# Kernel tuning notes

Measured on AMD Instinct MI355X. Metric: run time of the kernel, lower is better.

## Reference

```python
import jax, jax.numpy as jnp
import numpy as np

N_LAYER = 4
N_EMBD = 768
N_HEAD = 12
B, T = 4, 1024  # T = 4 * t, t = 256 (block_size)
EPS = 1e-5


def layernorm(x, g, b):
    mu = jnp.mean(x, axis=-1, keepdims=True)
    var = jnp.var(x, axis=-1, keepdims=True)
    return (x - mu) * jax.lax.rsqrt(var + EPS) * g + b


def setup_inputs() -> dict:
    key = jax.random.key(0)
    ks = jax.random.split(key, 20)
    C, L, H = N_EMBD, N_LAYER, 4 * N_EMBD
    std = 0.02
    inp = {
        "x": jax.random.normal(ks[0], (B, T, C), dtype=jnp.float32),
        "ln1_g": jnp.ones((L, C), jnp.float32),
        "ln1_b": jnp.zeros((L, C), jnp.float32),
        "Wq": std * jax.random.normal(ks[1], (L, C, C), jnp.float32),
        "bq": jnp.zeros((L, C), jnp.float32),
        "Wk": std * jax.random.normal(ks[2], (L, C, C), jnp.float32),
        "bk": jnp.zeros((L, C), jnp.float32),
        "Wv": std * jax.random.normal(ks[3], (L, C, C), jnp.float32),
        "bv": jnp.zeros((L, C), jnp.float32),
        "Wp": std * jax.random.normal(ks[4], (L, C, C), jnp.float32),
        "bp": jnp.zeros((L, C), jnp.float32),
        "ln2_g": jnp.ones((L, C), jnp.float32),
        "ln2_b": jnp.zeros((L, C), jnp.float32),
        "W1": std * jax.random.normal(ks[5], (L, C, H), jnp.float32),
        "b1": jnp.zeros((L, H), jnp.float32),
        "W2": std * jax.random.normal(ks[6], (L, H, C), jnp.float32),
        "b2": jnp.zeros((L, C), jnp.float32),
    }
    return inp


def _forward(x, ln1_g, ln1_b, Wq, bq, Wk, bk, Wv, bv, Wp, bp, ln2_g, ln2_b, W1, b1, W2, b2):
    Bx, Tx, C = x.shape
    hd = C // N_HEAD
    t = Tx // 4
    # cross-conditional mask: causal tril(t,t) tiled 4x4 over the 4 streams
    mask = jnp.tile(jnp.tril(jnp.ones((t, t), dtype=bool)), (4, 4))  # [T, T]
    scale = 1.0 / np.sqrt(hd).astype(np.float32)

    def block(h, p):
        (g1, b1g, wq, bqv, wk, bkv, wv, bvv, wp, bpv, g2, b2g, w1, b1v, w2, b2v) = p
        a_in = layernorm(h, g1, b1g)
        q = (a_in @ wq + bqv).reshape(Bx, Tx, N_HEAD, hd).transpose(0, 2, 1, 3)
        k = (a_in @ wk + bkv).reshape(Bx, Tx, N_HEAD, hd).transpose(0, 2, 1, 3)
        v = (a_in @ wv + bvv).reshape(Bx, Tx, N_HEAD, hd).transpose(0, 2, 1, 3)
        att = jnp.einsum('bhqd,bhkd->bhqk', q, k) * scale
        att = jnp.where(mask, att, -jnp.inf)
        att = jax.nn.softmax(att, axis=-1)
        y = jnp.einsum('bhqk,bhkd->bhqd', att, v)
        y = y.transpose(0, 2, 1, 3).reshape(Bx, Tx, C)
        h = h + (y @ wp + bpv)
        m_in = layernorm(h, g2, b2g)
        m = jax.nn.gelu(m_in @ w1 + b1v, approximate=False) @ w2 + b2v
        return h + m, None

    params = (ln1_g, ln1_b, Wq, bq, Wk, bk, Wv, bv, Wp, bp, ln2_g, ln2_b, W1, b1, W2, b2)
    x, _ = jax.lax.scan(block, x, params)
    return x


def reference(x, ln1_g, ln1_b, Wq, bq, Wk, bk, Wv, bv, Wp, bp, ln2_g, ln2_b, W1, b1, W2, b2):
    return _forward(x, ln1_g, ln1_b, Wq, bq, Wk, bk, Wv, bv, Wp, bp, ln2_g, ln2_b, W1, b1, W2, b2)
```

## Files before the change

### kernel.cpp

```cpp
#include <hip/hip_runtime.h>
#include <hip/hip_bf16.h>
#include <math.h>

typedef __hip_bfloat16 bf16;
typedef __attribute__((ext_vector_type(8))) short bf16x8;
typedef __attribute__((ext_vector_type(4))) float f32x4;

#define CDIM 768
#define HDIM 64
#define NHEAD 12
#define TSEQ 1024
#define MROWS 4096
#define HID 3072
#define QKVN 2304

__device__ inline void gld16(const void* g, void* l) {
  __builtin_amdgcn_global_load_lds((const __attribute__((address_space(1))) void*)g,
                                   (__attribute__((address_space(3))) void*)l, 16, 0, 0);
}

__global__ void k_transall(const float* __restrict__ Wq, const float* __restrict__ Wk,
                           const float* __restrict__ Wv, const float* __restrict__ Wp,
                           const float* __restrict__ W1, const float* __restrict__ W2,
                           const float* __restrict__ bq, const float* __restrict__ bk,
                           const float* __restrict__ bv,
                           bf16* __restrict__ wqkv, bf16* __restrict__ wtp,
                           bf16* __restrict__ wt1, bf16* __restrict__ wt2,
                           float* __restrict__ bqkv) {
  __shared__ float t[32][33];
  int blk = blockIdx.x;
  if (blk >= 6912) {
    int i = (blk - 6912) * 256 + threadIdx.y * 32 + threadIdx.x;
    if (i < QKVN) bqkv[i] = (i < CDIM) ? bq[i] : (i < 2 * CDIM) ? bk[i - CDIM] : bv[i - 2 * CDIM];
    return;
  }
  const float* src; bf16* dst; int K, N, n0, k0;
  if (blk < 1728) {
    int w = blk / 576, id = blk % 576;
    src = (w == 0) ? Wq : (w == 1) ? Wk : Wv;
    dst = wqkv + (size_t)w * CDIM * CDIM;
    K = CDIM; N = CDIM;
    n0 = (id % 24) * 32; k0 = (id / 24) * 32;
  } else if (blk < 2304) {
    int id = blk - 1728;
    src = Wp; dst = wtp; K = CDIM; N = CDIM;
    n0 = (id % 24) * 32; k0 = (id / 24) * 32;
  } else if (blk < 4608) {
    int id = blk - 2304;
    src = W1; dst = wt1; K = CDIM; N = HID;
    n0 = (id % 96) * 32; k0 = (id / 96) * 32;
  } else {
    int id = blk - 4608;
    src = W2; dst = wt2; K = HID; N = CDIM;
    n0 = (id % 24) * 32; k0 = (id / 24) * 32;
  }
  int c = threadIdx.x, ry = threadIdx.y;
  #pragma unroll
  for (int i = 0; i < 4; i++) {
    int r = ry + 8 * i;
    t[r][c] = src[(size_t)(k0 + r) * N + n0 + c];
  }
  __syncthreads();
  #pragma unroll
  for (int i = 0; i < 4; i++) {
    int r = ry + 8 * i;
    dst[(size_t)(n0 + r) * K + k0 + c] = __float2bfloat16(t[c][r]);
  }
}

__global__ __launch_bounds__(256) void k_ln(const float* __restrict__ h, const float* __restrict__ g,
                                            const float* __restrict__ b, bf16* __restrict__ out) {
  int row = blockIdx.x, tid = threadIdx.x;
  const float* hr = h + (size_t)row * CDIM;
  float x0 = hr[tid], x1 = hr[tid + 256], x2 = hr[tid + 512];
  float s = x0 + x1 + x2;
  float ss = x0 * x0 + x1 * x1 + x2 * x2;
  #pragma unroll
  for (int off = 32; off > 0; off >>= 1) {
    s  += __shfl_down(s, off, 64);
    ss += __shfl_down(ss, off, 64);
  }
  __shared__ float rs[4], rq[4];
  if ((tid & 63) == 0) { rs[tid >> 6] = s; rq[tid >> 6] = ss; }
  __syncthreads();
  s  = rs[0] + rs[1] + rs[2] + rs[3];
  ss = rq[0] + rq[1] + rq[2] + rq[3];
  float mu = s * (1.0f / CDIM);
  float var = ss * (1.0f / CDIM) - mu * mu;
  float rstd = rsqrtf(var + 1e-5f);
  bf16* orow = out + (size_t)row * CDIM;
  orow[tid]       = __float2bfloat16((x0 - mu) * rstd * g[tid]       + b[tid]);
  orow[tid + 256] = __float2bfloat16((x1 - mu) * rstd * g[tid + 256] + b[tid + 256]);
  orow[tid + 512] = __float2bfloat16((x2 - mu) * rstd * g[tid + 512] + b[tid + 512]);
}


template <int BM, int BN, int EPI>
__global__ __launch_bounds__(256) void k_gemmT(const bf16* __restrict__ A, const bf16* __restrict__ Bt,
                                               const float* __restrict__ bias,
                                               void* __restrict__ outv, int M, int N, int K) {
  constexpr int MR = BM / 32, NR = BN / 32;
  __shared__ __align__(16) bf16 As[BM * 64];
  __shared__ __align__(16) bf16 Bs[BN * 64];
  int tid = threadIdx.x;
  int m0 = blockIdx.x * BM, n0 = blockIdx.y * BN;
  int wave = tid >> 6, lane = tid & 63;
  int wr = wave >> 1, wc = wave & 1;
  int lrow = lane & 15, quad = lane >> 4;
  int sw = lrow & 7;
  f32x4 zz = {0.f, 0.f, 0.f, 0.f};
  f32x4 acc[MR][NR];
  #pragma unroll
  for (int i = 0; i < MR; i++)
    #pragma unroll
    for (int j = 0; j < NR; j++) acc[i][j] = zz;
  const bf16* Ag = A + (size_t)m0 * K;
  const bf16* Bg = Bt + (size_t)n0 * K;
  for (int k0 = 0; k0 < K; k0 += 64) {
    __syncthreads();
    #pragma unroll
    for (int i = 0; i < BM / 32; i++) {
      int idx = i * 256 + tid;
      int row = idx >> 3, c = idx & 7;
      gld16(Ag + (size_t)row * K + k0 + ((c ^ (row & 7)) * 8), As + idx * 8);
    }
    #pragma unroll
    for (int i = 0; i < BN / 32; i++) {
      int idx = i * 256 + tid;
      int row = idx >> 3, c = idx & 7;
      gld16(Bg + (size_t)row * K + k0 + ((c ^ (row & 7)) * 8), Bs + idx * 8);
    }
    __syncthreads();
    #pragma unroll
    for (int kc = 0; kc < 2; kc++) {
      int g = kc * 4 + quad;
      bf16x8 af[MR], bfr[NR];
      #pragma unroll
      for (int mi = 0; mi < MR; mi++)
        af[mi] = *(const bf16x8*)(As + (wr * (BM / 2) + mi * 16 + lrow) * 64 + ((g ^ sw) * 8));
      #pragma unroll
      for (int ni = 0; ni < NR; ni++)
        bfr[ni] = *(const bf16x8*)(Bs + (wc * (BN / 2) + ni * 16 + lrow) * 64 + ((g ^ sw) * 8));
      #pragma unroll
      for (int mi = 0; mi < MR; mi++)
        #pragma unroll
        for (int ni = 0; ni < NR; ni++)
          acc[mi][ni] = __builtin_amdgcn_mfma_f32_16x16x32_bf16(af[mi], bfr[ni], acc[mi][ni], 0, 0, 0);
    }
  }
  #pragma unroll
  for (int ni = 0; ni < NR; ni++) {
    int gc = n0 + wc * (BN / 2) + ni * 16 + lrow;
    float bval = bias[gc];
    #pragma unroll
    for (int mi = 0; mi < MR; mi++) {
      #pragma unroll
      for (int r = 0; r < 4; r++) {
        int grow = m0 + wr * (BM / 2) + mi * 16 + quad * 4 + r;
        float vv = acc[mi][ni][r] + bval;
        if (EPI == 1) vv = 0.5f * vv * (1.0f + erff(vv * 0.70710678118654752f));
        if (EPI == 2) {
          float* hp = (float*)outv + (size_t)grow * N + gc;
          *hp = *hp + vv;
        } else {
          ((bf16*)outv)[(size_t)grow * N + gc] = __float2bfloat16(vv);
        }
      }
    }
  }
}

__global__ __launch_bounds__(256) void k_attn(const bf16* __restrict__ qkv, bf16* __restrict__ y) {
  int bh = blockIdx.x;
  int b = bh / NHEAD, hh = bh % NHEAD;
  int qc = blockIdx.y;
  int tid = threadIdx.x;
  int wave = tid >> 6, lane = tid & 63;
  int lrow = lane & 15, quad = lane >> 4;
  int sw = lrow & 7;
  int q0 = qc * 64 + wave * 16;
  int qmod = q0 & 255;
  int qcmod = (qc * 64) & 255;

  const size_t rstride = QKVN;
  const bf16* qbase = qkv + (size_t)(b * TSEQ) * rstride + hh * HDIM;
  const bf16* kbase = qbase + CDIM;
  const bf16* vbase = qbase + 2 * CDIM;

  bf16x8 qf[2];
  #pragma unroll
  for (int kc = 0; kc < 2; kc++)
    qf[kc] = *(const bf16x8*)(qbase + (size_t)(q0 + lrow) * rstride + kc * 32 + quad * 8);

  f32x4 zz = {0.f, 0.f, 0.f, 0.f};
  f32x4 Oacc[4];
  #pragma unroll
  for (int j = 0; j < 4; j++) Oacc[j] = zz;
  float m[4] = {-1e30f, -1e30f, -1e30f, -1e30f};
  float l[4] = {0.f, 0.f, 0.f, 0.f};

  __shared__ __align__(16) bf16 Ks[64 * 64];
  __shared__ __align__(16) bf16 Vt[64 * 72];
  __shared__ __align__(16) bf16 Pl[4][16 * 64];

  for (int kt = 0; kt < 16; kt++) {
    int k0 = kt * 64;
    int kmod = k0 & 255;
    if (kmod > qcmod + 63) continue;
    __syncthreads();
    #pragma unroll
    for (int i = 0; i < 2; i++) {
      int idx = i * 256 + tid;
      int key = idx >> 3, c = idx & 7;
      gld16(kbase + (size_t)(k0 + key) * rstride + ((c ^ (key & 7)) * 8), Ks + idx * 8);
      int vkey = idx & 63, vd0 = (idx >> 6) * 8;
      bf16x8 vv = *(const bf16x8*)(vbase + (size_t)(k0 + vkey) * rstride + vd0);
      const bf16* vp = (const bf16*)&vv;
      #pragma unroll
      for (int j = 0; j < 8; j++) Vt[(vd0 + j) * 72 + vkey] = vp[j];
    }
    __syncthreads();
    if (kmod > qmod + 15) continue;

    f32x4 s[4];
    #pragma unroll
    for (int sub = 0; sub < 4; sub++) {
      s[sub] = zz;
      #pragma unroll
      for (int kc = 0; kc < 2; kc++) {
        int g = kc * 4 + quad;
        bf16x8 kf = *(const bf16x8*)(Ks + (sub * 16 + lrow) * 64 + ((g ^ sw) * 8));
        s[sub] = __builtin_amdgcn_mfma_f32_16x16x32_bf16(qf[kc], kf, s[sub], 0, 0, 0);
      }
    }
    bool partial = (kmod + 63 > qmod);
    #pragma unroll
    for (int sub = 0; sub < 4; sub++)
      #pragma unroll
      for (int r = 0; r < 4; r++) {
        float sv = s[sub][r] * 0.125f;
        if (partial) {
          int krel = kmod + sub * 16 + lrow;
          int qrel = qmod + quad * 4 + r;
          if (krel > qrel) sv = -1e30f;
        }
        s[sub][r] = sv;
      }
    float pr[4][4], alpha[4];
    #pragma unroll
    for (int r = 0; r < 4; r++) {
      float v = fmaxf(fmaxf(s[0][r], s[1][r]), fmaxf(s[2][r], s[3][r]));
      v = fmaxf(v, __shfl_xor(v, 1, 64));
      v = fmaxf(v, __shfl_xor(v, 2, 64));
      v = fmaxf(v, __shfl_xor(v, 4, 64));
      v = fmaxf(v, __shfl_xor(v, 8, 64));
      float mnew = fmaxf(m[r], v);
      alpha[r] = __expf(m[r] - mnew);
      m[r] = mnew;
      float rsum = 0.f;
      #pragma unroll
      for (int sub = 0; sub < 4; sub++) {
        pr[sub][r] = __expf(s[sub][r] - mnew);
        rsum += pr[sub][r];
      }
      rsum += __shfl_xor(rsum, 1, 64);
      rsum += __shfl_xor(rsum, 2, 64);
      rsum += __shfl_xor(rsum, 4, 64);
      rsum += __shfl_xor(rsum, 8, 64);
      l[r] = l[r] * alpha[r] + rsum;
    }
    #pragma unroll
    for (int j = 0; j < 4; j++)
      #pragma unroll
      for (int r = 0; r < 4; r++) Oacc[j][r] *= alpha[r];
    bf16* Pw = (bf16*)Pl[wave];
    #pragma unroll
    for (int sub = 0; sub < 4; sub++) {
      int cc = sub * 2 + (lrow >> 3);
      int e = lrow & 7;
      #pragma unroll
      for (int r = 0; r < 4; r++) {
        int mm = quad * 4 + r;
        Pw[mm * 64 + ((cc ^ (mm & 7)) * 8) + e] = __float2bfloat16(pr[sub][r]);
      }
    }
    bf16x8 pf[2];
    #pragma unroll
    for (int kc = 0; kc < 2; kc++) {
      int g = kc * 4 + quad;
      pf[kc] = *(const bf16x8*)(Pw + lrow * 64 + ((g ^ sw) * 8));
    }
    #pragma unroll
    for (int j = 0; j < 4; j++)
      #pragma unroll
      for (int kc = 0; kc < 2; kc++) {
        bf16x8 vf = *(const bf16x8*)(Vt + (j * 16 + lrow) * 72 + kc * 32 + quad * 8);
        Oacc[j] = __builtin_amdgcn_mfma_f32_16x16x32_bf16(pf[kc], vf, Oacc[j], 0, 0, 0);
      }
  }
  #pragma unroll
  for (int r = 0; r < 4; r++) {
    float inv = 1.0f / l[r];
    bf16* yp = y + (size_t)(b * TSEQ + q0 + quad * 4 + r) * CDIM + hh * HDIM;
    #pragma unroll
    for (int j = 0; j < 4; j++)
      yp[j * 16 + lrow] = __float2bfloat16(Oacc[j][r] * inv);
  }
}

extern "C" void kernel_launch(void* const* d_in, const int* in_sizes, int n_in,
                              void* d_out, int out_size, void* d_ws, size_t ws_size,
                              hipStream_t stream) {
  const float* x    = (const float*)d_in[0];
  const float* ln1g = (const float*)d_in[1];
  const float* ln1b = (const float*)d_in[2];
  const float* Wq   = (const float*)d_in[3];
  const float* bq   = (const float*)d_in[4];
  const float* Wk   = (const float*)d_in[5];
  const float* bk   = (const float*)d_in[6];
  const float* Wv   = (const float*)d_in[7];
  const float* bv   = (const float*)d_in[8];
  const float* Wp   = (const float*)d_in[9];
  const float* bp   = (const float*)d_in[10];
  const float* ln2g = (const float*)d_in[11];
  const float* ln2b = (const float*)d_in[12];
  const float* W1   = (const float*)d_in[13];
  const float* b1   = (const float*)d_in[14];
  const float* W2   = (const float*)d_in[15];
  const float* b2   = (const float*)d_in[16];

  char* ws = (char*)d_ws;
  size_t off = 0;
  float* h    = (float*)(ws + off); off += (size_t)MROWS * CDIM * 4;
  bf16* a     = (bf16*)(ws + off);  off += (size_t)MROWS * CDIM * 2;
  bf16* qkvb  = (bf16*)(ws + off);  off += (size_t)MROWS * QKVN * 2;
  bf16* yb    = (bf16*)(ws + off);  off += (size_t)MROWS * CDIM * 2;
  bf16* m1    = qkvb;
  bf16* wqkv  = (bf16*)(ws + off);  off += (size_t)QKVN * CDIM * 2;
  bf16* wtp   = (bf16*)(ws + off);  off += (size_t)CDIM * CDIM * 2;
  bf16* wt1   = (bf16*)(ws + off);  off += (size_t)CDIM * HID * 2;
  bf16* wt2   = (bf16*)(ws + off);  off += (size_t)CDIM * HID * 2;
  float* bqkv = (float*)(ws + off); off += (size_t)QKVN * 4;

  int n = MROWS * CDIM;
  hipMemcpyAsync(h, x, (size_t)n * sizeof(float), hipMemcpyDeviceToDevice, stream);

  for (int l = 0; l < 4; l++) {
    const float* Wql = Wq + (size_t)l * CDIM * CDIM;
    const float* Wkl = Wk + (size_t)l * CDIM * CDIM;
    const float* Wvl = Wv + (size_t)l * CDIM * CDIM;
    const float* Wpl = Wp + (size_t)l * CDIM * CDIM;
    const float* W1l = W1 + (size_t)l * CDIM * HID;
    const float* W2l = W2 + (size_t)l * HID * CDIM;

    k_transall<<<dim3(6921), dim3(32, 8), 0, stream>>>(Wql, Wkl, Wvl, Wpl, W1l, W2l,
                                                       bq + l * CDIM, bk + l * CDIM, bv + l * CDIM,
                                                       wqkv, wtp, wt1, wt2, bqkv);

    k_ln<<<dim3(MROWS), dim3(256), 0, stream>>>(h, ln1g + l * CDIM, ln1b + l * CDIM, a);

    k_gemmT<128, 128, 0><<<dim3(MROWS / 128, QKVN / 128), dim3(256), 0, stream>>>(
        a, wqkv, bqkv, qkvb, MROWS, QKVN, CDIM);

    k_attn<<<dim3(4 * NHEAD, 16), dim3(256), 0, stream>>>(qkvb, yb);

    k_gemmT<64, 64, 2><<<dim3(MROWS / 64, CDIM / 64), dim3(256), 0, stream>>>(
        yb, wtp, bp + (size_t)l * CDIM, h, MROWS, CDIM, CDIM);

    k_ln<<<dim3(MROWS), dim3(256), 0, stream>>>(h, ln2g + l * CDIM, ln2b + l * CDIM, a);

    k_gemmT<128, 128, 1><<<dim3(MROWS / 128, HID / 128), dim3(256), 0, stream>>>(
        a, wt1, b1 + (size_t)l * HID, m1, MROWS, HID, CDIM);

    k_gemmT<64, 64, 2><<<dim3(MROWS / 64, CDIM / 64), dim3(256), 0, stream>>>(
        m1, wt2, b2 + (size_t)l * CDIM, h, MROWS, CDIM, HID);
  }

  hipMemcpyAsync(d_out, h, (size_t)n * sizeof(float), hipMemcpyDeviceToDevice, stream);
}
```

Measured before the change: 928.2 us.

## Hoist weight transposes into one launch, vectorize layernorm, shrink GEMM M-tile

All four layers' weight transpose and bf16 conversion now run in a single launch before the layer loop when workspace allows, replacing one launch per layer. Layernorm now handles one row per wave with float4 loads and shuffle-xor reductions, dropping the shared-memory reduction and block sync. The QKV and MLP-up GEMMs switch from 128x128 to 64x128 tiles, doubling block count for better CU occupancy. The cost is more workspace for per-layer transposed weights and smaller tiles with less operand reuse.

Result: faster. 881.1 us (-5.1%).

```diff
diff --git a/kernel.cpp b/kernel.cpp
--- a/kernel.cpp
+++ b/kernel.cpp
@@ -4,6 +4,7 @@
 
 typedef __hip_bfloat16 bf16;
 typedef __attribute__((ext_vector_type(8))) short bf16x8;
+typedef __attribute__((ext_vector_type(4))) short s16x4;
 typedef __attribute__((ext_vector_type(4))) float f32x4;
 
 #define CDIM 768
@@ -18,17 +19,26 @@
   __builtin_amdgcn_global_load_lds((const __attribute__((address_space(1))) void*)g,
                                    (__attribute__((address_space(3))) void*)l, 16, 0, 0);
 }
-
-__global__ void k_transall(const float* __restrict__ Wq, const float* __restrict__ Wk,
-                           const float* __restrict__ Wv, const float* __restrict__ Wp,
-                           const float* __restrict__ W1, const float* __restrict__ W2,
-                           const float* __restrict__ bq, const float* __restrict__ bk,
-                           const float* __restrict__ bv,
-                           bf16* __restrict__ wqkv, bf16* __restrict__ wtp,
-                           bf16* __restrict__ wt1, bf16* __restrict__ wt2,
-                           float* __restrict__ bqkv) {
+__device__ inline short f2bs(float f) { bf16 h = __float2bfloat16(f); return *reinterpret_cast<short*>(&h); }
+
+__global__ void k_trans(const float* __restrict__ Wq, const float* __restrict__ Wk,
+                        const float* __restrict__ Wv, const float* __restrict__ Wp,
+                        const float* __restrict__ W1, const float* __restrict__ W2,
+                        const float* __restrict__ bq, const float* __restrict__ bk,
+                        const float* __restrict__ bv,
+                        bf16* __restrict__ wqkv, bf16* __restrict__ wtp,
+                        bf16* __restrict__ wt1, bf16* __restrict__ wt2,
+                        float* __restrict__ bqkv) {
   __shared__ float t[32][33];
   int blk = blockIdx.x;
+  int l = blk / 6921; blk -= l * 6921;
+  Wq += (size_t)l * CDIM * CDIM; Wk += (size_t)l * CDIM * CDIM;
+  Wv += (size_t)l * CDIM * CDIM; Wp += (size_t)l * CDIM * CDIM;
+  W1 += (size_t)l * CDIM * HID;  W2 += (size_t)l * HID * CDIM;
+  bq += (size_t)l * CDIM; bk += (size_t)l * CDIM; bv += (size_t)l * CDIM;
+  wqkv += (size_t)l * QKVN * CDIM; wtp += (size_t)l * CDIM * CDIM;
+  wt1  += (size_t)l * CDIM * HID;  wt2 += (size_t)l * CDIM * HID;
+  bqkv += (size_t)l * QKVN;
   if (blk >= 6912) {
     int i = (blk - 6912) * 256 + threadIdx.y * 32 + threadIdx.x;
     if (i < QKVN) bqkv[i] = (i < CDIM) ? bq[i] : (i < 2 * CDIM) ? bk[i - CDIM] : bv[i - 2 * CDIM];
@@ -70,28 +80,38 @@
 
 __global__ __launch_bounds__(256) void k_ln(const float* __restrict__ h, const float* __restrict__ g,
                                             const float* __restrict__ b, bf16* __restrict__ out) {
-  int row = blockIdx.x, tid = threadIdx.x;
-  const float* hr = h + (size_t)row * CDIM;
-  float x0 = hr[tid], x1 = hr[tid + 256], x2 = hr[tid + 512];
-  float s = x0 + x1 + x2;
-  float ss = x0 * x0 + x1 * x1 + x2 * x2;
+  int wave = threadIdx.x >> 6, lane = threadIdx.x & 63;
+  int row = blockIdx.x * 4 + wave;
+  const float4* hr = (const float4*)(h + (size_t)row * CDIM);
+  float4 v[3];
+  float s = 0.f, ss = 0.f;
+  #pragma unroll
+  for (int i = 0; i < 3; i++) {
+    v[i] = hr[lane * 3 + i];
+    s  += v[i].x + v[i].y + v[i].z + v[i].w;
+    ss += v[i].x * v[i].x + v[i].y * v[i].y + v[i].z * v[i].z + v[i].w * v[i].w;
+  }
   #pragma unroll
   for (int off = 32; off > 0; off >>= 1) {
-    s  += __shfl_down(s, off, 64);
-    ss += __shfl_down(ss, off, 64);
-  }
-  __shared__ float rs[4], rq[4];
-  if ((tid & 63) == 0) { rs[tid >> 6] = s; rq[tid >> 6] = ss; }
-  __syncthreads();
-  s  = rs[0] + rs[1] + rs[2] + rs[3];
-  ss = rq[0] + rq[1] + rq[2] + rq[3];
+    s  += __shfl_xor(s, off, 64);
+    ss += __shfl_xor(ss, off, 64);
+  }
   float mu = s * (1.0f / CDIM);
   float var = ss * (1.0f / CDIM) - mu * mu;
   float rstd = rsqrtf(var + 1e-5f);
-  bf16* orow = out + (size_t)row * CDIM;
-  orow[tid]       = __float2bfloat16((x0 - mu) * rstd * g[tid]       + b[tid]);
-  orow[tid + 256] = __float2bfloat16((x1 - mu) * rstd * g[tid + 256] + b[tid + 256]);
-  orow[tid + 512] = __float2bfloat16((x2 - mu) * rstd * g[tid + 512] + b[tid + 512]);
+  const float4* gp = (const float4*)g;
+  const float4* bp = (const float4*)b;
+  s16x4* orow = (s16x4*)(out + (size_t)row * CDIM);
+  #pragma unroll
+  for (int i = 0; i < 3; i++) {
+    float4 gg = gp[lane * 3 + i], bb = bp[lane * 3 + i];
+    s16x4 o;
+    o.x = f2bs((v[i].x - mu) * rstd * gg.x + bb.x);
+    o.y = f2bs((v[i].y - mu) * rstd * gg.y + bb.y);
+    o.z = f2bs((v[i].z - mu) * rstd * gg.z + bb.z);
+    o.w = f2bs((v[i].w - mu) * rstd * gg.w + bb.w);
+    orow[lane * 3 + i] = o;
+  }
 }
 
 
@@ -336,44 +356,61 @@
   bf16* qkvb  = (bf16*)(ws + off);  off += (size_t)MROWS * QKVN * 2;
   bf16* yb    = (bf16*)(ws + off);  off += (size_t)MROWS * CDIM * 2;
   bf16* m1    = qkvb;
-  bf16* wqkv  = (bf16*)(ws + off);  off += (size_t)QKVN * CDIM * 2;
-  bf16* wtp   = (bf16*)(ws + off);  off += (size_t)CDIM * CDIM * 2;
-  bf16* wt1   = (bf16*)(ws + off);  off += (size_t)CDIM * HID * 2;
-  bf16* wt2   = (bf16*)(ws + off);  off += (size_t)CDIM * HID * 2;
-  float* bqkv = (float*)(ws + off); off += (size_t)QKVN * 4;
+
+  const size_t szQkv = (size_t)QKVN * CDIM * 2;
+  const size_t szP   = (size_t)CDIM * CDIM * 2;
+  const size_t szW1  = (size_t)CDIM * HID * 2;
+  const size_t szW2  = (size_t)CDIM * HID * 2;
+  const size_t szB   = (size_t)QKVN * 4;
+  const size_t wlayer = szQkv + szP + szW1 + szW2 + szB;
+  bool hoist = ws_size >= off + 4 * wlayer + 4096;
+  int nW = hoist ? 4 : 1;
+
+  bf16* wqkv  = (bf16*)(ws + off);  off += nW * szQkv;
+  bf16* wtp   = (bf16*)(ws + off);  off += nW * szP;
+  bf16* wt1   = (bf16*)(ws + off);  off += nW * szW1;
+  bf16* wt2   = (bf16*)(ws + off);  off += nW * szW2;
+  float* bqkv = (float*)(ws + off); off += nW * szB;
 
   int n = MROWS * CDIM;
   hipMemcpyAsync(h, x, (size_t)n * sizeof(float), hipMemcpyDeviceToDevice, stream);
 
+  if (hoist)
+    k_trans<<<dim3(4 * 6921), dim3(32, 8), 0, stream>>>(Wq, Wk, Wv, Wp, W1, W2, bq, bk, bv,
+                                                        wqkv, wtp, wt1, wt2, bqkv);
+
   for (int l = 0; l < 4; l++) {
-    const float* Wql = Wq + (size_t)l * CDIM * CDIM;
-    const float* Wkl = Wk + (size_t)l * CDIM * CDIM;
-    const float* Wvl = Wv + (size_t)l * CDIM * CDIM;
-    const float* Wpl = Wp + (size_t)l * CDIM * CDIM;
-    const float* W1l = W1 + (size_t)l * CDIM * HID;
-    const float* W2l = W2 + (size_t)l * HID * CDIM;
-
-    k_transall<<<dim3(6921), dim3(32, 8), 0, stream>>>(Wql, Wkl, Wvl, Wpl, W1l, W2l,
-                                                       bq + l * CDIM, bk + l * CDIM, bv + l * CDIM,
-                                                       wqkv, wtp, wt1, wt2, bqkv);
-
-    k_ln<<<dim3(MROWS), dim3(256), 0, stream>>>(h, ln1g + l * CDIM, ln1b + l * CDIM, a);
-
-    k_gemmT<128, 128, 0><<<dim3(MROWS / 128, QKVN / 128), dim3(256), 0, stream>>>(
-        a, wqkv, bqkv, qkvb, MROWS, QKVN, CDIM);
+    int wl = hoist ? l : 0;
+    if (!hoist)
+      k_trans<<<dim3(6921), dim3(32, 8), 0, stream>>>(
+          Wq + (size_t)l * CDIM * CDIM, Wk + (size_t)l * CDIM * CDIM,
+          Wv + (size_t)l * CDIM * CDIM, Wp + (size_t)l * CDIM * CDIM,
+          W1 + (size_t)l * CDIM * HID, W2 + (size_t)l * HID * CDIM,
+          bq + (size_t)l * CDIM, bk + (size_t)l * CDIM, bv + (size_t)l * CDIM,
+          wqkv, wtp, wt1, wt2, bqkv);
+    const bf16* wqkvl = wqkv + (size_t)wl * QKVN * CDIM;
+    const bf16* wtpl  = wtp  + (size_t)wl * CDIM * CDIM;
+    const bf16* wt1l  = wt1  + (size_t)wl * CDIM * HID;
+    const bf16* wt2l  = wt2  + (size_t)wl * CDIM * HID;
+    const float* bqkvl = bqkv + (size_t)wl * QKVN;
+
+    k_ln<<<dim3(MROWS / 4), dim3(256), 0, stream>>>(h, ln1g + l * CDIM, ln1b + l * CDIM, a);
+
+    k_gemmT<64, 128, 0><<<dim3(MROWS / 64, QKVN / 128), dim3(256), 0, stream>>>(
+        a, wqkvl, bqkvl, qkvb, MROWS, QKVN, CDIM);
 
     k_attn<<<dim3(4 * NHEAD, 16), dim3(256), 0, stream>>>(qkvb, yb);
 
     k_gemmT<64, 64, 2><<<dim3(MROWS / 64, CDIM / 64), dim3(256), 0, stream>>>(
-        yb, wtp, bp + (size_t)l * CDIM, h, MROWS, CDIM, CDIM);
-
-    k_ln<<<dim3(MROWS), dim3(256), 0, stream>>>(h, ln2g + l * CDIM, ln2b + l * CDIM, a);
-
-    k_gemmT<128, 128, 1><<<dim3(MROWS / 128, HID / 128), dim3(256), 0, stream>>>(
-        a, wt1, b1 + (size_t)l * HID, m1, MROWS, HID, CDIM);
+        yb, wtpl, bp + (size_t)l * CDIM, h, MROWS, CDIM, CDIM);
+
+    k_ln<<<dim3(MROWS / 4), dim3(256), 0, stream>>>(h, ln2g + l * CDIM, ln2b + l * CDIM, a);
+
+    k_gemmT<64, 128, 1><<<dim3(MROWS / 64, HID / 128), dim3(256), 0, stream>>>(
+        a, wt1l, b1 + (size_t)l * HID, m1, MROWS, HID, CDIM);
 
     k_gemmT<64, 64, 2><<<dim3(MROWS / 64, CDIM / 64), dim3(256), 0, stream>>>(
-        m1, wt2, b2 + (size_t)l * CDIM, h, MROWS, CDIM, HID);
+        m1, wt2l, b2 + (size_t)l * CDIM, h, MROWS, CDIM, HID);
   }
 
   hipMemcpyAsync(d_out, h, (size_t)n * sizeof(float), hipMemcpyDeviceToDevice, stream);
```
